# Kernel optimization log

Hardware: AMD Instinct MI355X
Metric: run time of the kernel (lower is better)

The kernel has to match this reference:

```python
import jax, jax.numpy as jnp
import numpy as np

ALPHA = 0.2  # LeakyReLU negative slope
NEG_INF = -9e15


def setup_inputs() -> dict:
    key = jax.random.key(0)
    k_h, k_adj, k_W, k_a = jax.random.split(key, 4)
    N, d_in, d_out = 8192, 512, 64
    h = jax.random.normal(k_h, (N, d_in), dtype=jnp.float32)
    adj = jax.random.randint(k_adj, (N, N), 0, 2, dtype=jnp.int32)
    W = jax.random.normal(k_W, (d_in, d_out), dtype=jnp.float32) * (1.414 * (6.0 / (d_in + d_out)) ** 0.5)
    a = jax.random.normal(k_a, (2 * d_out, 1), dtype=jnp.float32) * (1.414 * (6.0 / (2 * d_out + 1)) ** 0.5)
    bias = jnp.zeros((d_out,), dtype=jnp.float32)
    return {"h": h, "adj": adj, "W": W, "a": a, "bias": bias}


def reference(h, adj, W, a, bias):
    d_out = W.shape[1]
    Wh = h @ W  # [N, d_out]
    # Additive decomposition of the concat-based score:
    # e_ij = LeakyReLU([Wh_i || Wh_j] @ a) = LeakyReLU(Wh_i@a1 + Wh_j@a2)
    a1 = a[:d_out, 0]  # [d_out]
    a2 = a[d_out:, 0]  # [d_out]
    s1 = Wh @ a1  # [N]
    s2 = Wh @ a2  # [N]
    e = s1[:, None] + s2[None, :]  # [N, N]
    e = jnp.where(e > 0, e, ALPHA * e)  # LeakyReLU
    e = jnp.where(adj > 0, e, NEG_INF)  # adjacency mask
    attention = jax.nn.softmax(e, axis=1)  # [N, N]
    h_prime = attention @ Wh + bias  # [N, d_out]
    return jax.nn.elu(h_prime)  # concat=True branch
```

## Files before the change

kernel.cpp:

```cpp
#include <hip/hip_runtime.h>
#include <stdint.h>

#define N_NODES 8192
#define D_IN    512
#define D_OUT   64
#define GAT_ALPHA 0.2f
#define S2_UB   44.0f

typedef __attribute__((ext_vector_type(8))) short short8v;
typedef __attribute__((ext_vector_type(4))) float f32x4;

__device__ __forceinline__ unsigned short f2bf_rne(float f) {
    unsigned u = __float_as_uint(f);
    unsigned r = u + 0x7FFFu + ((u >> 16) & 1u);
    return (unsigned short)(r >> 16);
}
__device__ __forceinline__ float bf2f(unsigned short s) {
    return __uint_as_float(((unsigned)s) << 16);
}

__global__ __launch_bounds__(256) void k_wh(
    const float* __restrict__ h, const float* __restrict__ W,
    const float* __restrict__ a, unsigned short* __restrict__ WhT,
    float* __restrict__ s1, float* __restrict__ s2)
{
    const int lane = threadIdx.x & 63;
    const int wv   = threadIdx.x >> 6;
    const int i    = blockIdx.x * 4 + wv;

    const float* hrow = h + (size_t)i * D_IN;
    float acc = 0.f;
#pragma unroll 8
    for (int k = 0; k < D_IN; k += 4) {
        const float4 h4 = *(const float4*)(hrow + k);
        acc = fmaf(h4.x, W[(k + 0) * D_OUT + lane], acc);
        acc = fmaf(h4.y, W[(k + 1) * D_OUT + lane], acc);
        acc = fmaf(h4.z, W[(k + 2) * D_OUT + lane], acc);
        acc = fmaf(h4.w, W[(k + 3) * D_OUT + lane], acc);
    }
    WhT[(size_t)lane * N_NODES + i] = f2bf_rne(acc);

    float p1 = acc * a[lane];
    float p2 = acc * a[D_OUT + lane];
#pragma unroll
    for (int off = 32; off; off >>= 1) {
        p1 += __shfl_xor(p1, off, 64);
        p2 += __shfl_xor(p2, off, 64);
    }
    if (lane == 0) {
        s1[i] = p1;
        s2[i] = p2;
    }
}

__global__ __launch_bounds__(512) void k_attn(
    const int* __restrict__ adj, const unsigned short* __restrict__ WhT,
    const float* __restrict__ s1, const float* __restrict__ s2,
    const float* __restrict__ bias, float* __restrict__ out)
{
    __shared__ int   adj_lds[16][260];
    __shared__ float s2_lds[256];
    __shared__ float num_lds[8][16][D_OUT];
    __shared__ float den_lds[8][16];

    const int tid = threadIdx.x;
    const int w   = tid >> 6;
    const int l   = tid & 63;
    const int r   = l & 15;
    const int kg  = l >> 4;
    const int i0  = blockIdx.x * 16;
    const int i   = i0 + r;

    const int srow = tid >> 5;
    const int scol = (tid & 31) * 8;
    const int* gsrc = adj + (size_t)(i0 + srow) * N_NODES + scol;

    const float s1r = s1[i];
    const float x0  = s1r + S2_UB;
    const float m   = fmaxf(x0, GAT_ALPHA * x0);

    f32x4 acc[4] = {};
    float den = 0.f;

    const int ccol = w * 32 + kg * 8;
    const unsigned short* wt0 = WhT + (size_t)(0 * 16 + r) * N_NODES + ccol;
    const unsigned short* wt1 = WhT + (size_t)(1 * 16 + r) * N_NODES + ccol;
    const unsigned short* wt2 = WhT + (size_t)(2 * 16 + r) * N_NODES + ccol;
    const unsigned short* wt3 = WhT + (size_t)(3 * 16 + r) * N_NODES + ccol;

    int4 rA = *(const int4*)(gsrc);
    int4 rB = *(const int4*)(gsrc + 4);
    float4 rS;
    if (tid < 64) rS = *(const float4*)(s2 + tid * 4);

    for (int mt = 0; mt < 32; ++mt) {
        const int jbase = mt * 256;

        *(int4*)&adj_lds[srow][scol]     = rA;
        *(int4*)&adj_lds[srow][scol + 4] = rB;
        if (tid < 64) *(float4*)&s2_lds[tid * 4] = rS;
        __syncthreads();

        if (mt + 1 < 32) {
            rA = *(const int4*)(gsrc + (mt + 1) * 256);
            rB = *(const int4*)(gsrc + (mt + 1) * 256 + 4);
            if (tid < 64) rS = *(const float4*)(s2 + jbase + 256 + tid * 4);
        }

        const int4   aA = *(const int4*)&adj_lds[r][ccol];
        const int4   aB = *(const int4*)&adj_lds[r][ccol + 4];
        const float4 sA = *(const float4*)&s2_lds[ccol];
        const float4 sB = *(const float4*)&s2_lds[ccol + 4];
        const short8v b0 = *(const short8v*)(wt0 + jbase);
        const short8v b1 = *(const short8v*)(wt1 + jbase);
        const short8v b2 = *(const short8v*)(wt2 + jbase);
        const short8v b3 = *(const short8v*)(wt3 + jbase);

        const float s2v[8] = { sA.x, sA.y, sA.z, sA.w, sB.x, sB.y, sB.z, sB.w };
        const int   av[8]  = { aA.x, aA.y, aA.z, aA.w, aB.x, aB.y, aB.z, aB.w };

        short8v af;
#pragma unroll
        for (int e = 0; e < 8; e++) {
            const float x  = s1r + s2v[e];
            const float xl = fmaxf(x, GAT_ALPHA * x);
            const float p  = (av[e] > 0) ? __expf(xl - m) : 0.f;
            const unsigned short q = f2bf_rne(p);
            af[e] = (short)q;
            den += bf2f(q);
        }

        acc[0] = __builtin_amdgcn_mfma_f32_16x16x32_bf16(af, b0, acc[0], 0, 0, 0);
        acc[1] = __builtin_amdgcn_mfma_f32_16x16x32_bf16(af, b1, acc[1], 0, 0, 0);
        acc[2] = __builtin_amdgcn_mfma_f32_16x16x32_bf16(af, b2, acc[2], 0, 0, 0);
        acc[3] = __builtin_amdgcn_mfma_f32_16x16x32_bf16(af, b3, acc[3], 0, 0, 0);

        __syncthreads();
    }

    den += __shfl_xor(den, 16, 64);
    den += __shfl_xor(den, 32, 64);

#pragma unroll
    for (int c = 0; c < 4; c++)
#pragma unroll
        for (int q = 0; q < 4; q++)
            num_lds[w][kg * 4 + q][c * 16 + r] = acc[c][q];
    if (l < 16) den_lds[w][l] = den;
    __syncthreads();

#pragma unroll
    for (int rep = 0; rep < 2; rep++) {
        const int eidx = rep * 512 + tid;
        const int il = eidx >> 6, o = eidx & 63;
        float nsum = 0.f, dsum = 0.f;
#pragma unroll
        for (int ww = 0; ww < 8; ww++) {
            nsum += num_lds[ww][il][o];
            dsum += den_lds[ww][il];
        }
        if (dsum == 0.f) dsum = 1.f;
        const float v = nsum / dsum + bias[o];
        out[(size_t)(i0 + il) * D_OUT + o] = v > 0.f ? v : expm1f(v);
    }
}

extern "C" void kernel_launch(void* const* d_in, const int* in_sizes, int n_in,
                              void* d_out, int out_size, void* d_ws, size_t ws_size,
                              hipStream_t stream)
{
    const float* h    = (const float*)d_in[0];
    const int*   adj  = (const int*)d_in[1];
    const float* W    = (const float*)d_in[2];
    const float* a    = (const float*)d_in[3];
    const float* bias = (const float*)d_in[4];
    float* out = (float*)d_out;

    char* ws = (char*)d_ws;
    unsigned short* WhT = (unsigned short*)ws;
    float*          s1  = (float*)(ws + (size_t)1 * 1024 * 1024);
    float*          s2  = s1 + N_NODES;

    k_wh<<<N_NODES / 4, 256, 0, stream>>>(h, W, a, WhT, s1, s2);
    k_attn<<<N_NODES / 16, 512, 0, stream>>>(adj, WhT, s1, s2, bias, out);
}
```

Measured before the change: 160.6 us.

## Split attention over two column halves with double-buffered LDS and finalize kernel

The attention kernel now splits the neighbor (column) dimension into two halves, doubling the grid to 1024 blocks. Each block writes partial numerators and denominators to workspace, and a new finalize kernel combines them and applies bias and ELU. The adjacency and s2 staging buffers are double-buffered in LDS, which removes the trailing barrier in each iteration. This is meant to raise occupancy and parallelism on a 256-CU device. In exchange it adds an extra launch and about 4 MB of partial-result traffic.

```diff
diff --git a/kernel.cpp b/kernel.cpp
--- a/kernel.cpp
+++ b/kernel.cpp
@@ -56,24 +56,26 @@
 __global__ __launch_bounds__(512) void k_attn(
     const int* __restrict__ adj, const unsigned short* __restrict__ WhT,
     const float* __restrict__ s1, const float* __restrict__ s2,
-    const float* __restrict__ bias, float* __restrict__ out)
-{
-    __shared__ int   adj_lds[16][260];
-    __shared__ float s2_lds[256];
-    __shared__ float num_lds[8][16][D_OUT];
-    __shared__ float den_lds[8][16];
+    float* __restrict__ num2, float* __restrict__ den2)
+{
+    __shared__ char smem[2 * 16 * 260 * 4 + 2 * 256 * 4];
+    int   (*adj_lds)[16][260] = (int(*)[16][260])smem;
+    float (*s2_lds)[256]      = (float(*)[256])(smem + 2 * 16 * 260 * 4);
 
     const int tid = threadIdx.x;
     const int w   = tid >> 6;
     const int l   = tid & 63;
     const int r   = l & 15;
     const int kg  = l >> 4;
-    const int i0  = blockIdx.x * 16;
+    const int bid = blockIdx.x;
+    const int jh  = bid & 1;
+    const int i0  = (bid >> 1) * 16;
     const int i   = i0 + r;
+    const int jb0 = jh * 4096;
 
     const int srow = tid >> 5;
     const int scol = (tid & 31) * 8;
-    const int* gsrc = adj + (size_t)(i0 + srow) * N_NODES + scol;
+    const int* gsrc = adj + (size_t)(i0 + srow) * N_NODES + jb0 + scol;
 
     const float s1r = s1[i];
     const float x0  = s1r + S2_UB;
@@ -83,38 +85,39 @@
     float den = 0.f;
 
     const int ccol = w * 32 + kg * 8;
-    const unsigned short* wt0 = WhT + (size_t)(0 * 16 + r) * N_NODES + ccol;
-    const unsigned short* wt1 = WhT + (size_t)(1 * 16 + r) * N_NODES + ccol;
-    const unsigned short* wt2 = WhT + (size_t)(2 * 16 + r) * N_NODES + ccol;
-    const unsigned short* wt3 = WhT + (size_t)(3 * 16 + r) * N_NODES + ccol;
+    const unsigned short* wt0 = WhT + (size_t)(0 * 16 + r) * N_NODES + jb0 + ccol;
+    const unsigned short* wt1 = WhT + (size_t)(1 * 16 + r) * N_NODES + jb0 + ccol;
+    const unsigned short* wt2 = WhT + (size_t)(2 * 16 + r) * N_NODES + jb0 + ccol;
+    const unsigned short* wt3 = WhT + (size_t)(3 * 16 + r) * N_NODES + jb0 + ccol;
 
     int4 rA = *(const int4*)(gsrc);
     int4 rB = *(const int4*)(gsrc + 4);
     float4 rS;
-    if (tid < 64) rS = *(const float4*)(s2 + tid * 4);
-
-    for (int mt = 0; mt < 32; ++mt) {
-        const int jbase = mt * 256;
-
-        *(int4*)&adj_lds[srow][scol]     = rA;
-        *(int4*)&adj_lds[srow][scol + 4] = rB;
-        if (tid < 64) *(float4*)&s2_lds[tid * 4] = rS;
+    if (tid < 64) rS = *(const float4*)(s2 + jb0 + tid * 4);
+
+    for (int t = 0; t < 16; ++t) {
+        const int buf = t & 1;
+        const int jt  = t * 256;
+
+        *(int4*)&adj_lds[buf][srow][scol]     = rA;
+        *(int4*)&adj_lds[buf][srow][scol + 4] = rB;
+        if (tid < 64) *(float4*)&s2_lds[buf][tid * 4] = rS;
         __syncthreads();
 
-        if (mt + 1 < 32) {
-            rA = *(const int4*)(gsrc + (mt + 1) * 256);
-            rB = *(const int4*)(gsrc + (mt + 1) * 256 + 4);
-            if (tid < 64) rS = *(const float4*)(s2 + jbase + 256 + tid * 4);
+        if (t + 1 < 16) {
+            rA = *(const int4*)(gsrc + (t + 1) * 256);
+            rB = *(const int4*)(gsrc + (t + 1) * 256 + 4);
+            if (tid < 64) rS = *(const float4*)(s2 + jb0 + jt + 256 + tid * 4);
         }
 
-        const int4   aA = *(const int4*)&adj_lds[r][ccol];
-        const int4   aB = *(const int4*)&adj_lds[r][ccol + 4];
-        const float4 sA = *(const float4*)&s2_lds[ccol];
-        const float4 sB = *(const float4*)&s2_lds[ccol + 4];
-        const short8v b0 = *(const short8v*)(wt0 + jbase);
-        const short8v b1 = *(const short8v*)(wt1 + jbase);
-        const short8v b2 = *(const short8v*)(wt2 + jbase);
-        const short8v b3 = *(const short8v*)(wt3 + jbase);
+        const int4   aA = *(const int4*)&adj_lds[buf][r][ccol];
+        const int4   aB = *(const int4*)&adj_lds[buf][r][ccol + 4];
+        const float4 sA = *(const float4*)&s2_lds[buf][ccol];
+        const float4 sB = *(const float4*)&s2_lds[buf][ccol + 4];
+        const short8v b0 = *(const short8v*)(wt0 + jt);
+        const short8v b1 = *(const short8v*)(wt1 + jt);
+        const short8v b2 = *(const short8v*)(wt2 + jt);
+        const short8v b3 = *(const short8v*)(wt3 + jt);
 
         const float s2v[8] = { sA.x, sA.y, sA.z, sA.w, sB.x, sB.y, sB.z, sB.w };
         const int   av[8]  = { aA.x, aA.y, aA.z, aA.w, aB.x, aB.y, aB.z, aB.w };
@@ -134,12 +137,14 @@
         acc[1] = __builtin_amdgcn_mfma_f32_16x16x32_bf16(af, b1, acc[1], 0, 0, 0);
         acc[2] = __builtin_amdgcn_mfma_f32_16x16x32_bf16(af, b2, acc[2], 0, 0, 0);
         acc[3] = __builtin_amdgcn_mfma_f32_16x16x32_bf16(af, b3, acc[3], 0, 0, 0);
-
-        __syncthreads();
     }
 
     den += __shfl_xor(den, 16, 64);
     den += __shfl_xor(den, 32, 64);
+
+    __syncthreads();
+    float (*num_lds)[16][D_OUT] = (float(*)[16][D_OUT])smem;
+    float (*den_lds)[16]        = (float(*)[16])(smem + 8 * 16 * D_OUT * 4);
 
 #pragma unroll
     for (int c = 0; c < 4; c++)
@@ -159,10 +164,37 @@
             nsum += num_lds[ww][il][o];
             dsum += den_lds[ww][il];
         }
-        if (dsum == 0.f) dsum = 1.f;
-        const float v = nsum / dsum + bias[o];
-        out[(size_t)(i0 + il) * D_OUT + o] = v > 0.f ? v : expm1f(v);
-    }
+        num2[((size_t)jh * N_NODES + i0 + il) * D_OUT + o] = nsum;
+        if (o == 0) den2[(size_t)jh * N_NODES + i0 + il] = dsum;
+    }
+}
+
+__global__ __launch_bounds__(256) void k_fin(
+    const float* __restrict__ num2, const float* __restrict__ den2,
+    const float* __restrict__ bias, float* __restrict__ out)
+{
+    const size_t idx4 = (size_t)blockIdx.x * 256 + threadIdx.x;
+    const size_t base = idx4 * 4;
+    const size_t i = base >> 6;
+    const int    o = (int)(base & 63);
+
+    const float4 n0 = *(const float4*)(num2 + i * D_OUT + o);
+    const float4 n1 = *(const float4*)(num2 + ((size_t)N_NODES + i) * D_OUT + o);
+    float d = den2[i] + den2[N_NODES + i];
+    if (d == 0.f) d = 1.f;
+    const float inv = 1.f / d;
+    const float4 b4 = *(const float4*)(bias + o);
+
+    float4 v;
+    v.x = (n0.x + n1.x) * inv + b4.x;
+    v.y = (n0.y + n1.y) * inv + b4.y;
+    v.z = (n0.z + n1.z) * inv + b4.z;
+    v.w = (n0.w + n1.w) * inv + b4.w;
+    v.x = v.x > 0.f ? v.x : expm1f(v.x);
+    v.y = v.y > 0.f ? v.y : expm1f(v.y);
+    v.z = v.z > 0.f ? v.z : expm1f(v.z);
+    v.w = v.w > 0.f ? v.w : expm1f(v.w);
+    *(float4*)(out + base) = v;
 }
 
 extern "C" void kernel_launch(void* const* d_in, const int* in_sizes, int n_in,
@@ -177,10 +209,13 @@
     float* out = (float*)d_out;
 
     char* ws = (char*)d_ws;
-    unsigned short* WhT = (unsigned short*)ws;
-    float*          s1  = (float*)(ws + (size_t)1 * 1024 * 1024);
-    float*          s2  = s1 + N_NODES;
+    unsigned short* WhT  = (unsigned short*)ws;
+    float*          s1   = (float*)(ws + (size_t)1 * 1024 * 1024);
+    float*          s2   = s1 + N_NODES;
+    float*          num2 = (float*)(ws + (size_t)2 * 1024 * 1024);
+    float*          den2 = (float*)(ws + (size_t)6 * 1024 * 1024);
 
     k_wh<<<N_NODES / 4, 256, 0, stream>>>(h, W, a, WhT, s1, s2);
-    k_attn<<<N_NODES / 16, 512, 0, stream>>>(adj, WhT, s1, s2, bias, out);
-}
+    k_attn<<<(N_NODES / 16) * 2, 512, 0, stream>>>(adj, WhT, s1, s2, num2, den2);
+    k_fin<<<(N_NODES * D_OUT) / (256 * 4), 256, 0, stream>>>(num2, den2, bias, out);
+}
```

Measured after the change: 165.8 us. +3.3%, slower.
